# Kernel tuning notes

Measured on AMD Instinct MI355X. Metric: run time of the kernel, lower is better.

## Reference

```python
import jax, jax.numpy as jnp
import numpy as np

D = 512
H = 8
DK = D // H
EPS = 1e-5

def _layer_norm(x, w, b):
    mu = jnp.mean(x, axis=-1, keepdims=True)
    var = jnp.mean(jnp.square(x - mu), axis=-1, keepdims=True)
    return (x - mu) * jax.lax.rsqrt(var + EPS) * w + b

def setup_inputs() -> dict:
    key = jax.random.key(0)
    ks = jax.random.split(key, 16)
    B, S = 4, 2048
    s = 1.0 / np.sqrt(D)
    inp = {
        'q': jax.random.normal(ks[0], (B, S, D), jnp.float32),
        'k': jax.random.normal(ks[1], (B, S, D), jnp.float32),
        'v': jax.random.normal(ks[2], (B, S, D), jnp.float32),
        'mask': jnp.ones((S, S), jnp.int32),
        'pos_k': jax.random.normal(ks[3], (S, S), jnp.float32),
        'ln_w': jnp.ones((D,), jnp.float32),
        'ln_b': jnp.zeros((D,), jnp.float32),
        'Wq': jax.random.uniform(ks[4], (D, D), jnp.float32, -s, s),
        'bq': jax.random.uniform(ks[5], (D,), jnp.float32, -s, s),
        'Wk': jax.random.uniform(ks[6], (D, D), jnp.float32, -s, s),
        'bk': jax.random.uniform(ks[7], (D,), jnp.float32, -s, s),
        'Wv': jax.random.uniform(ks[8], (D, D), jnp.float32, -s, s),
        'bv': jax.random.uniform(ks[9], (D,), jnp.float32, -s, s),
        'Wo': jax.random.uniform(ks[10], (D, D), jnp.float32, -s, s),
        'bo': jax.random.uniform(ks[11], (D,), jnp.float32, -s, s),
    }
    return inp

def reference(q, k, v, mask, pos_k, ln_w, ln_b, Wq, bq, Wk, bk, Wv, bv, Wo, bo):
    B, S, _ = q.shape
    # shared LayerNorm on q, k, v
    qn = _layer_norm(q, ln_w, ln_b)
    kn = _layer_norm(k, ln_w, ln_b)
    vn = _layer_norm(v, ln_w, ln_b)
    # projections -> [B, H, S, DK]
    qh = (qn @ Wq.T + bq).reshape(B, S, H, DK).transpose(0, 2, 1, 3)
    kh = (kn @ Wk.T + bk).reshape(B, S, H, DK).transpose(0, 2, 1, 3)
    vh = (vn @ Wv.T + bv).reshape(B, S, H, DK).transpose(0, 2, 1, 3)
    scores = jnp.einsum('bhqd,bhkd->bhqk', qh, kh) / np.sqrt(DK)
    scores = scores + pos_k[None, None, :S, :S]
    scores = jnp.where(mask[None, None] == 0, -jnp.inf, scores)
    attn = jax.nn.softmax(scores, axis=-1)  # dropout is identity in eval
    x = jnp.einsum('bhqk,bhkd->bhqd', attn, vh).transpose(0, 2, 1, 3).reshape(B, S, D)
    out = x @ Wo.T + bo
    return out, attn
```

## Files before the change

### kernel.cpp

```cpp
#include <hip/hip_runtime.h>


typedef __bf16 bf16;
typedef __attribute__((ext_vector_type(8))) __bf16 bfv8;
typedef __attribute__((ext_vector_type(4))) __bf16 bfv4;
typedef __attribute__((ext_vector_type(2))) __bf16 bfv2;
typedef __attribute__((ext_vector_type(4))) float  f32x4;
typedef __attribute__((ext_vector_type(2))) float  f32x2;

static constexpr int Dm = 512, Hh = 8, Sq = 2048, Bb = 4;
static constexpr int BS = Bb * Sq;

__device__ __forceinline__ f32x4 mfma16(bfv8 a, bfv8 b, f32x4 c) {
  return __builtin_amdgcn_mfma_f32_16x16x32_bf16(a, b, c, 0, 0, 0);
}

__global__ __launch_bounds__(256) void posT_kernel(
    const float* __restrict__ pos, const int* __restrict__ mask,
    float* __restrict__ posT) {
  __shared__ float tile[32][33];
  int i0 = blockIdx.y * 32, j0 = blockIdx.x * 32;
  int tx = threadIdx.x & 31, ty = threadIdx.x >> 5;
#pragma unroll
  for (int rr = 0; rr < 32; rr += 8) {
    int i = i0 + ty + rr, j = j0 + tx;
    float pv = pos[(size_t)i * Sq + j];
    int   mv = mask[(size_t)i * Sq + j];
    tile[ty + rr][tx] = mv ? pv : -1e30f;
  }
  __syncthreads();
#pragma unroll
  for (int rr = 0; rr < 32; rr += 8) {
    int j = j0 + ty + rr, i = i0 + tx;
    posT[(size_t)j * Sq + i] = tile[tx][ty + rr];
  }
}

__global__ __launch_bounds__(256) void ln_kernel(
    const float* __restrict__ q, const float* __restrict__ k,
    const float* __restrict__ v, const float* __restrict__ w,
    const float* __restrict__ bia, bf16* __restrict__ qn,
    bf16* __restrict__ kn, bf16* __restrict__ vn) {
  int wv = threadIdx.x >> 6, lane = threadIdx.x & 63;
  int row = blockIdx.x * 4 + wv;
  int which = blockIdx.y;
  const float* src = which == 0 ? q : (which == 1 ? k : v);
  bf16* dst        = which == 0 ? qn : (which == 1 ? kn : vn);

  f32x4 x0 = *(const f32x4*)(src + (size_t)row * Dm + lane * 8);
  f32x4 x1 = *(const f32x4*)(src + (size_t)row * Dm + lane * 8 + 4);
  float xf[8], s1 = 0.f, s2 = 0.f;
#pragma unroll
  for (int i = 0; i < 4; i++) { xf[i] = x0[i]; xf[4 + i] = x1[i]; }
#pragma unroll
  for (int i = 0; i < 8; i++) { s1 += xf[i]; s2 += xf[i] * xf[i]; }
#pragma unroll
  for (int m = 1; m < 64; m <<= 1) { s1 += __shfl_xor(s1, m, 64); s2 += __shfl_xor(s2, m, 64); }
  float mu = s1 * (1.0f / 512.0f);
  float var = s2 * (1.0f / 512.0f) - mu * mu;
  float rs = rsqrtf(var + 1e-5f);
  f32x4 w0 = *(const f32x4*)(w + lane * 8);
  f32x4 w1 = *(const f32x4*)(w + lane * 8 + 4);
  f32x4 b0 = *(const f32x4*)(bia + lane * 8);
  f32x4 b1 = *(const f32x4*)(bia + lane * 8 + 4);
  bfv8 o;
#pragma unroll
  for (int i = 0; i < 4; i++) {
    o[i]     = (bf16)((xf[i] - mu) * rs * w0[i] + b0[i]);
    o[4 + i] = (bf16)((xf[4 + i] - mu) * rs * w1[i] + b1[i]);
  }
  *(bfv8*)(dst + (size_t)row * Dm + lane * 8) = o;
}

__device__ __forceinline__ void gemm_body(
    const bf16* __restrict__ A, const float* __restrict__ W,
    const float* __restrict__ bias, bf16* __restrict__ outb,
    float* __restrict__ outf, int mode, int m0, int n0) {
  __shared__ __align__(16) bf16 As[64][72];
  __shared__ __align__(16) bf16 Bs[64][72];
  int tid = threadIdx.x;
  int wv = tid >> 6, lane = tid & 63;
  int wm = (wv & 1) * 32, wn = (wv >> 1) * 32;
  int r16 = lane & 15, quad = lane >> 4;
  int lr = tid >> 2, sc = (tid & 3) * 16;

  f32x4 acc[2][2] = {};
  const bf16*  Ap = A + (size_t)(m0 + lr) * 512 + sc;
  const float* Wp = W + (size_t)(n0 + lr) * 512 + sc;

  for (int k0 = 0; k0 < 512; k0 += 64) {
    bfv8 a0 = *(const bfv8*)(Ap + k0);
    bfv8 a1 = *(const bfv8*)(Ap + k0 + 8);
    f32x4 w0 = *(const f32x4*)(Wp + k0);
    f32x4 w1 = *(const f32x4*)(Wp + k0 + 4);
    f32x4 w2 = *(const f32x4*)(Wp + k0 + 8);
    f32x4 w3 = *(const f32x4*)(Wp + k0 + 12);
    bfv8 bb0, bb1;
#pragma unroll
    for (int i = 0; i < 4; i++) {
      bb0[i] = (bf16)w0[i]; bb0[4 + i] = (bf16)w1[i];
      bb1[i] = (bf16)w2[i]; bb1[4 + i] = (bf16)w3[i];
    }
    __syncthreads();
    *(bfv8*)&As[lr][sc] = a0;  *(bfv8*)&As[lr][sc + 8] = a1;
    *(bfv8*)&Bs[lr][sc] = bb0; *(bfv8*)&Bs[lr][sc + 8] = bb1;
    __syncthreads();
#pragma unroll
    for (int kk = 0; kk < 2; kk++) {
      bfv8 af0 = *(const bfv8*)&As[wm + r16][kk * 32 + quad * 8];
      bfv8 af1 = *(const bfv8*)&As[wm + 16 + r16][kk * 32 + quad * 8];
      bfv8 bf0 = *(const bfv8*)&Bs[wn + r16][kk * 32 + quad * 8];
      bfv8 bf1 = *(const bfv8*)&Bs[wn + 16 + r16][kk * 32 + quad * 8];
      acc[0][0] = mfma16(af0, bf0, acc[0][0]);
      acc[0][1] = mfma16(af0, bf1, acc[0][1]);
      acc[1][0] = mfma16(af1, bf0, acc[1][0]);
      acc[1][1] = mfma16(af1, bf1, acc[1][1]);
    }
  }

#pragma unroll
  for (int nt = 0; nt < 2; nt++) {
    int n = n0 + wn + nt * 16 + r16;
    float bb = bias[n];
#pragma unroll
    for (int mt = 0; mt < 2; mt++) {
#pragma unroll
      for (int r = 0; r < 4; r++) {
        int m = m0 + wm + mt * 16 + quad * 4 + r;
        float o = acc[mt][nt][r] + bb;
        int bb_ = m >> 11, s = m & 2047, hh = n >> 6, dd = n & 63;
        if (mode == 0)
          outb[(((size_t)(bb_ * Hh + hh)) * Sq + s) * 64 + dd] = (bf16)o;
        else if (mode == 1)
          outb[(((size_t)(bb_ * Hh + hh)) * 64 + dd) * Sq + s] = (bf16)o;
        else
          outf[(size_t)m * 512 + n] = o;
      }
    }
  }
}

__global__ __launch_bounds__(256) void gemm_proj(
    const bf16* __restrict__ qn, const bf16* __restrict__ kn,
    const bf16* __restrict__ vn, const float* __restrict__ Wq,
    const float* __restrict__ Wk, const float* __restrict__ Wv,
    const float* __restrict__ bq, const float* __restrict__ bk,
    const float* __restrict__ bv, bf16* __restrict__ qhp,
    bf16* __restrict__ khp, bf16* __restrict__ vhT) {
  int z = blockIdx.z;
  const bf16*  A    = z == 0 ? qn : (z == 1 ? kn : vn);
  const float* W    = z == 0 ? Wq : (z == 1 ? Wk : Wv);
  const float* bias = z == 0 ? bq : (z == 1 ? bk : bv);
  bf16*        outb = z == 0 ? qhp : (z == 1 ? khp : vhT);
  int mode = (z == 2) ? 1 : 0;
  gemm_body(A, W, bias, outb, nullptr, mode, blockIdx.x * 64, blockIdx.y * 64);
}

__global__ __launch_bounds__(256) void gemm_bt(
    const bf16* __restrict__ A, const float* __restrict__ W,
    const float* __restrict__ bias, bf16* __restrict__ outb,
    float* __restrict__ outf, int mode) {
  gemm_body(A, W, bias, outb, outf, mode, blockIdx.x * 64, blockIdx.y * 64);
}

__global__ __launch_bounds__(512, 4) void attn_kernel(
    const bf16* __restrict__ qh, const bf16* __restrict__ kh,
    const bf16* __restrict__ vT, const float* __restrict__ posT,
    float* __restrict__ attn, bf16* __restrict__ xout) {
  __shared__ float smax[8][16];
  __shared__ float ssum[8][16];
  __shared__ __align__(16) char upool[8 * 16 * 136 * 2];
  auto Pbuf = reinterpret_cast<bf16(*)[16][136]>(upool);
  auto xred = reinterpret_cast<float(*)[16][64]>(upool);

  const int tid = threadIdx.x;
  const int wv = tid >> 6, lane = tid & 63;
  const int r16 = lane & 15, quad = lane >> 4;

  const int bid = blockIdx.x;
  const int nbid = (bid & 7) * 512 + (bid >> 3);
  const int bh = nbid >> 7;
  const int strip = nbid & 127;
  const int b = bh >> 3, h = bh & 7;
  const int r0 = strip * 16;
  const int c0 = wv * 256;

  const bf16* qbase = qh + (size_t)bh * Sq * 64;
  const bf16* kbase = kh + (size_t)bh * Sq * 64;
  const bf16* vbase = vT + (size_t)bh * 64 * Sq;

  bfv8 aq0 = *(const bfv8*)(qbase + (size_t)(r0 + r16) * 64 + quad * 8);
  bfv8 aq1 = *(const bfv8*)(qbase + (size_t)(r0 + r16) * 64 + 32 + quad * 8);

  f32x4 acc[16];
#pragma unroll
  for (int t = 0; t < 16; t++) {
    const bf16* kp = kbase + (size_t)(c0 + t * 16 + r16) * 64 + quad * 8;
    bfv8 kb0 = *(const bfv8*)kp;
    bfv8 kb1 = *(const bfv8*)(kp + 32);
    f32x4 z = {0.f, 0.f, 0.f, 0.f};
    z = mfma16(aq0, kb0, z);
    z = mfma16(aq1, kb1, z);
    acc[t] = z;
  }

  float mx[4] = {-1e30f, -1e30f, -1e30f, -1e30f};
#pragma unroll
  for (int t = 0; t < 16; t++) {
    int colg = c0 + t * 16 + r16;
    f32x4 pk = *(const f32x4*)(posT + (size_t)colg * Sq + r0 + quad * 4);
#pragma unroll
    for (int r = 0; r < 4; r++) {
      float s = acc[t][r] * 0.125f + pk[r];
      acc[t][r] = s;
      mx[r] = fmaxf(mx[r], s);
    }
  }
#pragma unroll
  for (int m = 1; m < 16; m <<= 1)
#pragma unroll
    for (int r = 0; r < 4; r++) mx[r] = fmaxf(mx[r], __shfl_xor(mx[r], m, 64));

  float sm[4] = {0.f, 0.f, 0.f, 0.f};
#pragma unroll
  for (int t = 0; t < 16; t++)
#pragma unroll
    for (int r = 0; r < 4; r++) {
      float e = __expf(acc[t][r] - mx[r]);
      acc[t][r] = e;
      sm[r] += e;
    }
#pragma unroll
  for (int m = 1; m < 16; m <<= 1)
#pragma unroll
    for (int r = 0; r < 4; r++) sm[r] += __shfl_xor(sm[r], m, 64);

  if (r16 == 0) {
#pragma unroll
    for (int r = 0; r < 4; r++) {
      smax[wv][quad * 4 + r] = mx[r];
      ssum[wv][quad * 4 + r] = sm[r];
    }
  }
  __syncthreads();

  float comb[4];
#pragma unroll
  for (int r = 0; r < 4; r++) {
    int row = quad * 4 + r;
    float M = smax[0][row];
#pragma unroll
    for (int w = 1; w < 8; w++) M = fmaxf(M, smax[w][row]);
    float S = 0.f;
#pragma unroll
    for (int w = 0; w < 8; w++) S += ssum[w][row] * __expf(smax[w][row] - M);
    comb[r] = __expf(mx[r] - M) / S;
  }

  f32x4 xacc[4] = {};
#pragma unroll
  for (int c = 0; c < 2; c++) {
#pragma unroll
    for (int tt = 0; tt < 8; tt++) {
      int t = c * 8 + tt;
      int colg = c0 + t * 16 + r16;
#pragma unroll
      for (int r = 0; r < 4; r++) {
        float p = acc[t][r] * comb[r];
        Pbuf[wv][quad * 4 + r][tt * 16 + r16] = (bf16)p;
        attn[((size_t)bh * Sq + r0 + quad * 4 + r) * Sq + colg] = p;
      }
    }
#pragma unroll
    for (int ks = 0; ks < 4; ks++) {
      bfv8 af = *(const bfv8*)&Pbuf[wv][r16][ks * 32 + quad * 8];
      int key0 = c0 + c * 128 + ks * 32;
#pragma unroll
      for (int nt = 0; nt < 4; nt++) {
        bfv8 bvv = *(const bfv8*)(vbase + (size_t)(nt * 16 + r16) * Sq + key0 + quad * 8);
        xacc[nt] = mfma16(af, bvv, xacc[nt]);
      }
    }
  }

  __syncthreads();
#pragma unroll
  for (int nt = 0; nt < 4; nt++)
#pragma unroll
    for (int r = 0; r < 4; r++)
      xred[wv][quad * 4 + r][nt * 16 + r16] = xacc[nt][r];
  __syncthreads();
  {
    int row = tid >> 5, d2 = (tid & 31) * 2;
    f32x2 s = {0.f, 0.f};
#pragma unroll
    for (int w = 0; w < 8; w++) s += *(const f32x2*)&xred[w][row][d2];
    bfv2 o;
    o[0] = (bf16)s[0];
    o[1] = (bf16)s[1];
    *(bfv2*)(xout + ((size_t)(b * Sq + r0 + row)) * 512 + h * 64 + d2) = o;
  }
}

extern "C" void kernel_launch(void* const* d_in, const int* in_sizes, int n_in,
                              void* d_out, int out_size, void* d_ws,
                              size_t ws_size, hipStream_t stream) {
  const float* q    = (const float*)d_in[0];
  const float* k    = (const float*)d_in[1];
  const float* v    = (const float*)d_in[2];
  const int*   mask = (const int*)d_in[3];
  const float* pos  = (const float*)d_in[4];
  const float* lnw  = (const float*)d_in[5];
  const float* lnb  = (const float*)d_in[6];
  const float* Wq   = (const float*)d_in[7];
  const float* bq   = (const float*)d_in[8];
  const float* Wk   = (const float*)d_in[9];
  const float* bk   = (const float*)d_in[10];
  const float* Wv   = (const float*)d_in[11];
  const float* bv   = (const float*)d_in[12];
  const float* Wo   = (const float*)d_in[13];
  const float* bo   = (const float*)d_in[14];

  const size_t NE = (size_t)Bb * Sq * Dm;
  if (ws_size < 64ull * 1024 * 1024) return;

  char* wsb = (char*)d_ws;
  float* posT = (float*)wsb;
  bf16* qn   = (bf16*)(wsb + 16ull * 1024 * 1024);
  bf16* kn   = (bf16*)(wsb + 24ull * 1024 * 1024);
  bf16* vn   = (bf16*)(wsb + 32ull * 1024 * 1024);
  bf16* qhp  = (bf16*)(wsb + 40ull * 1024 * 1024);
  bf16* khp  = (bf16*)(wsb + 48ull * 1024 * 1024);
  bf16* vhT  = (bf16*)(wsb + 56ull * 1024 * 1024);
  bf16* xbuf = qn;

  float* out  = (float*)d_out;
  float* attn = out + NE;

  posT_kernel<<<dim3(Sq / 32, Sq / 32), 256, 0, stream>>>(pos, mask, posT);
  ln_kernel<<<dim3(BS / 4, 3), 256, 0, stream>>>(q, k, v, lnw, lnb, qn, kn, vn);
  gemm_proj<<<dim3(BS / 64, Dm / 64, 3), 256, 0, stream>>>(
      qn, kn, vn, Wq, Wk, Wv, bq, bk, bv, qhp, khp, vhT);
  attn_kernel<<<dim3((Sq / 16) * Hh * Bb), 512, 0, stream>>>(qhp, khp, vhT,
                                                             posT, attn, xbuf);
  gemm_bt<<<dim3(BS / 64, Dm / 64), 256, 0, stream>>>(xbuf, Wo, bo, nullptr, out, 2);
}
```

Before: 947.4 us.

## Tile positional bias per strip and stage attn writes through LDS for vector stores

The masked positional bias is now stored in a strip-major layout (16 query rows contiguous per key column), so each attention block reads one contiguous chunk instead of striding across the transposed matrix. The attention-probability output, previously written as scattered scalar stores, is staged in a per-wave LDS tile and written back as coalesced 16-byte row segments. This targets the dominant fp32 attn write traffic and the bias reads. The cost is about 35KB of extra LDS per block, which may lower occupancy under the 4-blocks-per-CU launch bound.

```diff
diff --git a/kernel.cpp b/kernel.cpp
--- a/kernel.cpp
+++ b/kernel.cpp
@@ -15,9 +15,9 @@
   return __builtin_amdgcn_mfma_f32_16x16x32_bf16(a, b, c, 0, 0, 0);
 }
 
-__global__ __launch_bounds__(256) void posT_kernel(
+__global__ __launch_bounds__(256) void posS_kernel(
     const float* __restrict__ pos, const int* __restrict__ mask,
-    float* __restrict__ posT) {
+    float* __restrict__ posS) {
   __shared__ float tile[32][33];
   int i0 = blockIdx.y * 32, j0 = blockIdx.x * 32;
   int tx = threadIdx.x & 31, ty = threadIdx.x >> 5;
@@ -32,7 +32,7 @@
 #pragma unroll
   for (int rr = 0; rr < 32; rr += 8) {
     int j = j0 + ty + rr, i = i0 + tx;
-    posT[(size_t)j * Sq + i] = tile[tx][ty + rr];
+    posS[(size_t)((i >> 4) * Sq + j) * 16 + (i & 15)] = tile[tx][ty + rr];
   }
 }
 
@@ -165,13 +165,14 @@
 
 __global__ __launch_bounds__(512, 4) void attn_kernel(
     const bf16* __restrict__ qh, const bf16* __restrict__ kh,
-    const bf16* __restrict__ vT, const float* __restrict__ posT,
+    const bf16* __restrict__ vT, const float* __restrict__ posS,
     float* __restrict__ attn, bf16* __restrict__ xout) {
   __shared__ float smax[8][16];
   __shared__ float ssum[8][16];
   __shared__ __align__(16) char upool[8 * 16 * 136 * 2];
   auto Pbuf = reinterpret_cast<bf16(*)[16][136]>(upool);
   auto xred = reinterpret_cast<float(*)[16][64]>(upool);
+  __shared__ __align__(16) float Sst[8][16][68];
 
   const int tid = threadIdx.x;
   const int wv = tid >> 6, lane = tid & 63;
@@ -188,6 +189,7 @@
   const bf16* qbase = qh + (size_t)bh * Sq * 64;
   const bf16* kbase = kh + (size_t)bh * Sq * 64;
   const bf16* vbase = vT + (size_t)bh * 64 * Sq;
+  const float* pbase = posS + (size_t)strip * Sq * 16;
 
   bfv8 aq0 = *(const bfv8*)(qbase + (size_t)(r0 + r16) * 64 + quad * 8);
   bfv8 aq1 = *(const bfv8*)(qbase + (size_t)(r0 + r16) * 64 + 32 + quad * 8);
@@ -208,7 +210,7 @@
 #pragma unroll
   for (int t = 0; t < 16; t++) {
     int colg = c0 + t * 16 + r16;
-    f32x4 pk = *(const f32x4*)(posT + (size_t)colg * Sq + r0 + quad * 4);
+    f32x4 pk = *(const f32x4*)(pbase + (size_t)colg * 16 + quad * 4);
 #pragma unroll
     for (int r = 0; r < 4; r++) {
       float s = acc[t][r] * 0.125f + pk[r];
@@ -261,14 +263,24 @@
 #pragma unroll
   for (int c = 0; c < 2; c++) {
 #pragma unroll
-    for (int tt = 0; tt < 8; tt++) {
-      int t = c * 8 + tt;
-      int colg = c0 + t * 16 + r16;
-#pragma unroll
-      for (int r = 0; r < 4; r++) {
-        float p = acc[t][r] * comb[r];
-        Pbuf[wv][quad * 4 + r][tt * 16 + r16] = (bf16)p;
-        attn[((size_t)bh * Sq + r0 + quad * 4 + r) * Sq + colg] = p;
+    for (int half = 0; half < 2; half++) {
+#pragma unroll
+      for (int tt4 = 0; tt4 < 4; tt4++) {
+        int tt = half * 4 + tt4;
+        int t = c * 8 + tt;
+#pragma unroll
+        for (int r = 0; r < 4; r++) {
+          float p = acc[t][r] * comb[r];
+          Pbuf[wv][quad * 4 + r][tt * 16 + r16] = (bf16)p;
+          Sst[wv][quad * 4 + r][tt4 * 16 + r16] = p;
+        }
+      }
+      int colbase = c0 + c * 128 + half * 64;
+#pragma unroll
+      for (int pass = 0; pass < 4; pass++) {
+        int row = pass * 4 + quad;
+        f32x4 vv = *(const f32x4*)&Sst[wv][row][r16 * 4];
+        *(f32x4*)(attn + ((size_t)bh * Sq + r0 + row) * Sq + colbase + r16 * 4) = vv;
       }
     }
 #pragma unroll
@@ -325,7 +337,7 @@
   if (ws_size < 64ull * 1024 * 1024) return;
 
   char* wsb = (char*)d_ws;
-  float* posT = (float*)wsb;
+  float* posS = (float*)wsb;
   bf16* qn   = (bf16*)(wsb + 16ull * 1024 * 1024);
   bf16* kn   = (bf16*)(wsb + 24ull * 1024 * 1024);
   bf16* vn   = (bf16*)(wsb + 32ull * 1024 * 1024);
@@ -337,11 +349,11 @@
   float* out  = (float*)d_out;
   float* attn = out + NE;
 
-  posT_kernel<<<dim3(Sq / 32, Sq / 32), 256, 0, stream>>>(pos, mask, posT);
+  posS_kernel<<<dim3(Sq / 32, Sq / 32), 256, 0, stream>>>(pos, mask, posS);
   ln_kernel<<<dim3(BS / 4, 3), 256, 0, stream>>>(q, k, v, lnw, lnb, qn, kn, vn);
   gemm_proj<<<dim3(BS / 64, Dm / 64, 3), 256, 0, stream>>>(
       qn, kn, vn, Wq, Wk, Wv, bq, bk, bv, qhp, khp, vhT);
   attn_kernel<<<dim3((Sq / 16) * Hh * Bb), 512, 0, stream>>>(qhp, khp, vhT,
-                                                             posT, attn, xbuf);
+                                                             posS, attn, xbuf);
   gemm_bt<<<dim3(BS / 64, Dm / 64), 256, 0, stream>>>(xbuf, Wo, bo, nullptr, out, 2);
 }
```

Measured after the change: 932.0 us. About the same (-1.6%).

## Transpose QK^T MFMA so P stays in registers, drop LDS staging

Applied to the files above, without the earlier changes.

The QK^T MFMA operands are swapped so each lane holds four consecutive keys of one query row. The softmax probabilities can then feed the PV MFMA straight from registers, which removes the Pbuf LDS round-trip and one barrier. The attn output is now written as contiguous float4 stores per row. To match, the pos/mask table is re-laid out in a strip-tiled order, and the V transpose permutes keys within 32-key groups to fit the new register ordering. The risk is correctness if the key permutation does not match the MFMA operand layout.

```diff
diff --git a/kernel.cpp b/kernel.cpp
--- a/kernel.cpp
+++ b/kernel.cpp
@@ -15,9 +15,9 @@
   return __builtin_amdgcn_mfma_f32_16x16x32_bf16(a, b, c, 0, 0, 0);
 }
 
-__global__ __launch_bounds__(256) void posT_kernel(
+__global__ __launch_bounds__(256) void posQ_kernel(
     const float* __restrict__ pos, const int* __restrict__ mask,
-    float* __restrict__ posT) {
+    float* __restrict__ posQ) {
   __shared__ float tile[32][33];
   int i0 = blockIdx.y * 32, j0 = blockIdx.x * 32;
   int tx = threadIdx.x & 31, ty = threadIdx.x >> 5;
@@ -32,7 +32,8 @@
 #pragma unroll
   for (int rr = 0; rr < 32; rr += 8) {
     int j = j0 + ty + rr, i = i0 + tx;
-    posT[(size_t)j * Sq + i] = tile[tx][ty + rr];
+    posQ[(size_t)(i >> 4) * 32768 + (size_t)(j >> 2) * 64 + (i & 15) * 4 +
+         (j & 3)] = tile[tx][ty + rr];
   }
 }
 
@@ -129,12 +130,16 @@
         int m = m0 + wm + mt * 16 + quad * 4 + r;
         float o = acc[mt][nt][r] + bb;
         int bb_ = m >> 11, s = m & 2047, hh = n >> 6, dd = n & 63;
-        if (mode == 0)
+        if (mode == 0) {
           outb[(((size_t)(bb_ * Hh + hh)) * Sq + s) * 64 + dd] = (bf16)o;
-        else if (mode == 1)
-          outb[(((size_t)(bb_ * Hh + hh)) * 64 + dd) * Sq + s] = (bf16)o;
-        else
+        } else if (mode == 1) {
+          int local = s & 31;
+          int pos = ((local >> 2) & 3) * 8 + (local >> 4) * 4 + (local & 3);
+          int sp = (s & ~31) | pos;
+          outb[(((size_t)(bb_ * Hh + hh)) * 64 + dd) * Sq + sp] = (bf16)o;
+        } else {
           outf[(size_t)m * 512 + n] = o;
+        }
       }
     }
   }
@@ -165,13 +170,11 @@
 
 __global__ __launch_bounds__(512, 4) void attn_kernel(
     const bf16* __restrict__ qh, const bf16* __restrict__ kh,
-    const bf16* __restrict__ vT, const float* __restrict__ posT,
+    const bf16* __restrict__ vT, const float* __restrict__ posQ,
     float* __restrict__ attn, bf16* __restrict__ xout) {
   __shared__ float smax[8][16];
   __shared__ float ssum[8][16];
-  __shared__ __align__(16) char upool[8 * 16 * 136 * 2];
-  auto Pbuf = reinterpret_cast<bf16(*)[16][136]>(upool);
-  auto xred = reinterpret_cast<float(*)[16][64]>(upool);
+  __shared__ __align__(16) float xred[8][16][64];
 
   const int tid = threadIdx.x;
   const int wv = tid >> 6, lane = tid & 63;
@@ -188,6 +191,7 @@
   const bf16* qbase = qh + (size_t)bh * Sq * 64;
   const bf16* kbase = kh + (size_t)bh * Sq * 64;
   const bf16* vbase = vT + (size_t)bh * 64 * Sq;
+  const float* pbase = posQ + (size_t)strip * 32768;
 
   bfv8 aq0 = *(const bfv8*)(qbase + (size_t)(r0 + r16) * 64 + quad * 8);
   bfv8 aq1 = *(const bfv8*)(qbase + (size_t)(r0 + r16) * 64 + 32 + quad * 8);
@@ -199,91 +203,75 @@
     bfv8 kb0 = *(const bfv8*)kp;
     bfv8 kb1 = *(const bfv8*)(kp + 32);
     f32x4 z = {0.f, 0.f, 0.f, 0.f};
-    z = mfma16(aq0, kb0, z);
-    z = mfma16(aq1, kb1, z);
+    z = mfma16(kb0, aq0, z);
+    z = mfma16(kb1, aq1, z);
     acc[t] = z;
   }
 
-  float mx[4] = {-1e30f, -1e30f, -1e30f, -1e30f};
+  float mx = -1e30f;
 #pragma unroll
   for (int t = 0; t < 16; t++) {
-    int colg = c0 + t * 16 + r16;
-    f32x4 pk = *(const f32x4*)(posT + (size_t)colg * Sq + r0 + quad * 4);
+    f32x4 pk = *(const f32x4*)(pbase + (size_t)((c0 >> 2) + t * 4 + quad) * 64 +
+                               r16 * 4);
 #pragma unroll
     for (int r = 0; r < 4; r++) {
       float s = acc[t][r] * 0.125f + pk[r];
       acc[t][r] = s;
-      mx[r] = fmaxf(mx[r], s);
-    }
-  }
-#pragma unroll
-  for (int m = 1; m < 16; m <<= 1)
-#pragma unroll
-    for (int r = 0; r < 4; r++) mx[r] = fmaxf(mx[r], __shfl_xor(mx[r], m, 64));
-
-  float sm[4] = {0.f, 0.f, 0.f, 0.f};
+      mx = fmaxf(mx, s);
+    }
+  }
+  mx = fmaxf(mx, __shfl_xor(mx, 16, 64));
+  mx = fmaxf(mx, __shfl_xor(mx, 32, 64));
+
+  float sm = 0.f;
 #pragma unroll
   for (int t = 0; t < 16; t++)
 #pragma unroll
     for (int r = 0; r < 4; r++) {
-      float e = __expf(acc[t][r] - mx[r]);
+      float e = __expf(acc[t][r] - mx);
       acc[t][r] = e;
-      sm[r] += e;
-    }
-#pragma unroll
-  for (int m = 1; m < 16; m <<= 1)
-#pragma unroll
-    for (int r = 0; r < 4; r++) sm[r] += __shfl_xor(sm[r], m, 64);
-
-  if (r16 == 0) {
+      sm += e;
+    }
+  sm += __shfl_xor(sm, 16, 64);
+  sm += __shfl_xor(sm, 32, 64);
+
+  if (quad == 0) {
+    smax[wv][r16] = mx;
+    ssum[wv][r16] = sm;
+  }
+  __syncthreads();
+
+  float M = smax[0][r16];
+#pragma unroll
+  for (int w = 1; w < 8; w++) M = fmaxf(M, smax[w][r16]);
+  float S = 0.f;
+#pragma unroll
+  for (int w = 0; w < 8; w++) S += ssum[w][r16] * __expf(smax[w][r16] - M);
+  float comb = __expf(mx - M) / S;
+
+  float* arow = attn + ((size_t)bh * Sq + r0 + r16) * Sq;
+  f32x4 xacc[4] = {};
+#pragma unroll
+  for (int ks = 0; ks < 8; ks++) {
+    f32x4 p0, p1;
 #pragma unroll
     for (int r = 0; r < 4; r++) {
-      smax[wv][quad * 4 + r] = mx[r];
-      ssum[wv][quad * 4 + r] = sm[r];
-    }
-  }
-  __syncthreads();
-
-  float comb[4];
-#pragma unroll
-  for (int r = 0; r < 4; r++) {
-    int row = quad * 4 + r;
-    float M = smax[0][row];
-#pragma unroll
-    for (int w = 1; w < 8; w++) M = fmaxf(M, smax[w][row]);
-    float S = 0.f;
-#pragma unroll
-    for (int w = 0; w < 8; w++) S += ssum[w][row] * __expf(smax[w][row] - M);
-    comb[r] = __expf(mx[r] - M) / S;
-  }
-
-  f32x4 xacc[4] = {};
-#pragma unroll
-  for (int c = 0; c < 2; c++) {
-#pragma unroll
-    for (int tt = 0; tt < 8; tt++) {
-      int t = c * 8 + tt;
-      int colg = c0 + t * 16 + r16;
-#pragma unroll
-      for (int r = 0; r < 4; r++) {
-        float p = acc[t][r] * comb[r];
-        Pbuf[wv][quad * 4 + r][tt * 16 + r16] = (bf16)p;
-        attn[((size_t)bh * Sq + r0 + quad * 4 + r) * Sq + colg] = p;
-      }
-    }
-#pragma unroll
-    for (int ks = 0; ks < 4; ks++) {
-      bfv8 af = *(const bfv8*)&Pbuf[wv][r16][ks * 32 + quad * 8];
-      int key0 = c0 + c * 128 + ks * 32;
-#pragma unroll
-      for (int nt = 0; nt < 4; nt++) {
-        bfv8 bvv = *(const bfv8*)(vbase + (size_t)(nt * 16 + r16) * Sq + key0 + quad * 8);
-        xacc[nt] = mfma16(af, bvv, xacc[nt]);
-      }
-    }
-  }
-
-  __syncthreads();
+      p0[r] = acc[2 * ks][r] * comb;
+      p1[r] = acc[2 * ks + 1][r] * comb;
+    }
+    int key0 = c0 + ks * 32;
+    *(f32x4*)(arow + key0 + quad * 4) = p0;
+    *(f32x4*)(arow + key0 + 16 + quad * 4) = p1;
+    bfv8 pa;
+#pragma unroll
+    for (int r = 0; r < 4; r++) { pa[r] = (bf16)p0[r]; pa[4 + r] = (bf16)p1[r]; }
+#pragma unroll
+    for (int nt = 0; nt < 4; nt++) {
+      bfv8 bvv = *(const bfv8*)(vbase + (size_t)(nt * 16 + r16) * Sq + key0 + quad * 8);
+      xacc[nt] = mfma16(pa, bvv, xacc[nt]);
+    }
+  }
+
 #pragma unroll
   for (int nt = 0; nt < 4; nt++)
 #pragma unroll
@@ -325,7 +313,7 @@
   if (ws_size < 64ull * 1024 * 1024) return;
 
   char* wsb = (char*)d_ws;
-  float* posT = (float*)wsb;
+  float* posQ = (float*)wsb;
   bf16* qn   = (bf16*)(wsb + 16ull * 1024 * 1024);
   bf16* kn   = (bf16*)(wsb + 24ull * 1024 * 1024);
   bf16* vn   = (bf16*)(wsb + 32ull * 1024 * 1024);
@@ -337,11 +325,11 @@
   float* out  = (float*)d_out;
   float* attn = out + NE;
 
-  posT_kernel<<<dim3(Sq / 32, Sq / 32), 256, 0, stream>>>(pos, mask, posT);
+  posQ_kernel<<<dim3(Sq / 32, Sq / 32), 256, 0, stream>>>(pos, mask, posQ);
   ln_kernel<<<dim3(BS / 4, 3), 256, 0, stream>>>(q, k, v, lnw, lnb, qn, kn, vn);
   gemm_proj<<<dim3(BS / 64, Dm / 64, 3), 256, 0, stream>>>(
       qn, kn, vn, Wq, Wk, Wv, bq, bk, bv, qhp, khp, vhT);
   attn_kernel<<<dim3((Sq / 16) * Hh * Bb), 512, 0, stream>>>(qhp, khp, vhT,
-                                                             posT, attn, xbuf);
+                                                             posQ, attn, xbuf);
   gemm_bt<<<dim3(BS / 64, Dm / 64), 256, 0, stream>>>(xbuf, Wo, bo, nullptr, out, 2);
 }
```

Result: no change. 932.2 us (-1.6%).
